# Performance work log

Hardware: AMD Instinct MI355X
Metric: run time of the kernel (lower is better)

The kernel has to match this reference:

```python
import jax, jax.numpy as jnp
import numpy as np

B, S, D, H, T, R = 2, 2048, 768, 12, 64, 50
DH = D // H
EPS = 1e-12


def setup_inputs() -> dict:
    key = jax.random.key(0)
    ks = jax.random.split(key, 12)
    w = lambda k, shape: jax.random.normal(k, shape, jnp.float32) * 0.02
    inp = {
        "hidden_states": jax.random.normal(ks[0], (B, S, D), jnp.float32),
        "tag_emb": w(ks[1], (T, D)),
        "sa_wq": w(ks[2], (D, D)), "sa_bq": jnp.zeros((D,), jnp.float32),
        "sa_wk": w(ks[3], (D, D)), "sa_bk": jnp.zeros((D,), jnp.float32),
        "sa_wv": w(ks[4], (D, D)), "sa_bv": jnp.zeros((D,), jnp.float32),
        "sa_wo": w(ks[5], (D, D)), "sa_bo": jnp.zeros((D,), jnp.float32),
        "sa_ln_g": jnp.ones((D,), jnp.float32), "sa_ln_b": jnp.zeros((D,), jnp.float32),
        "ca_wq": w(ks[6], (D, D)), "ca_bq": jnp.zeros((D,), jnp.float32),
        "ca_wk": w(ks[7], (D, D)), "ca_bk": jnp.zeros((D,), jnp.float32),
        "ca_wv": w(ks[8], (D, D)), "ca_bv": jnp.zeros((D,), jnp.float32),
        "ca_wo": w(ks[9], (D, D)), "ca_bo": jnp.zeros((D,), jnp.float32),
        "ca_ln_g": jnp.ones((D,), jnp.float32), "ca_ln_b": jnp.zeros((D,), jnp.float32),
        "ff_w1": w(ks[10], (D, 3072)), "ff_b1": jnp.zeros((3072,), jnp.float32),
        "ff_w2": w(ks[11], (3072, D)), "ff_b2": jnp.zeros((D,), jnp.float32),
        "ff_ln_g": jnp.ones((D,), jnp.float32), "ff_ln_b": jnp.zeros((D,), jnp.float32),
    }
    return inp


def _layernorm(x, g, b):
    m = jnp.mean(x, axis=-1, keepdims=True)
    v = jnp.mean(jnp.square(x - m), axis=-1, keepdims=True)
    return (x - m) * jax.lax.rsqrt(v + EPS) * g + b


def _bert_attention(x, kv, mask, wq, bq, wk, bk, wv, bv, wo, bo, ln_g, ln_b):
    # BertSelfAttention: multi-head attn; mask (if any) is ADDED to scores (HF semantics).
    Bq, Sq = x.shape[0], x.shape[1]
    Sk = kv.shape[1]
    q = (x @ wq + bq).reshape(Bq, Sq, H, DH)
    k = (kv @ wk + bk).reshape(Bq, Sk, H, DH)
    v = (kv @ wv + bv).reshape(Bq, Sk, H, DH)
    scores = jnp.einsum("bqhd,bkhd->bhqk", q, k) / jnp.sqrt(jnp.float32(DH))
    if mask is not None:
        scores = scores + mask  # additive 0/1 band mask, as in the source
    probs = jax.nn.softmax(scores, axis=-1)
    ctx = jnp.einsum("bhqk,bkhd->bqhd", probs, v).reshape(Bq, Sq, D)
    # BertSelfOutput: dense + residual + LayerNorm
    return _layernorm(ctx @ wo + bo + x, ln_g, ln_b)


def reference(hidden_states, tag_emb,
              sa_wq, sa_bq, sa_wk, sa_bk, sa_wv, sa_bv, sa_wo, sa_bo, sa_ln_g, sa_ln_b,
              ca_wq, ca_bq, ca_wk, ca_bk, ca_wv, ca_bv, ca_wo, ca_bo, ca_ln_g, ca_ln_b,
              ff_w1, ff_b1, ff_w2, ff_b2, ff_ln_g, ff_ln_b):
    Sd = hidden_states.shape[1]
    # banded mask: tril(+R) * triu(-R) -> 1 inside window, 0 outside (added to scores)
    i = jnp.arange(Sd)
    band = (jnp.abs(i[:, None] - i[None, :]) <= R).astype(hidden_states.dtype)  # [S,S]
    attn_out = _bert_attention(hidden_states, hidden_states, band,
                               sa_wq, sa_bq, sa_wk, sa_bk, sa_wv, sa_bv,
                               sa_wo, sa_bo, sa_ln_g, sa_ln_b)
    tags = jnp.broadcast_to(tag_emb[None], (hidden_states.shape[0], T, D))
    attn_out = _bert_attention(attn_out, tags, None,
                               ca_wq, ca_bq, ca_wk, ca_bk, ca_wv, ca_bv,
                               ca_wo, ca_bo, ca_ln_g, ca_ln_b)
    # BertIntermediate + BertOutput (exact erf gelu as in HF)
    inter = jax.nn.gelu(attn_out @ ff_w1 + ff_b1, approximate=False)
    return _layernorm(inter @ ff_w2 + ff_b2 + attn_out, ff_ln_g, ff_ln_b)
```

## Files before the change

kernel.cpp:

```cpp
#include <hip/hip_runtime.h>
#include <cstdint>
#include <cstddef>


typedef __bf16 bf16;
typedef __bf16 bf16x8 __attribute__((ext_vector_type(8)));
typedef __bf16 bf16x4 __attribute__((ext_vector_type(4)));
typedef __bf16 bf16x2 __attribute__((ext_vector_type(2)));
typedef float  floatx4 __attribute__((ext_vector_type(4)));

__device__ __forceinline__ void glds16(const bf16* g, bf16* l) {
  __builtin_amdgcn_global_load_lds((const __attribute__((address_space(1))) void*)g,
                                   (__attribute__((address_space(3))) void*)l, 16, 0, 0);
}

__device__ __forceinline__ float fexp2(float x) {
  float r;
  asm("v_exp_f32 %0, %1" : "=v"(r) : "v"(x));
  return r;
}

__global__ __launch_bounds__(256) void k_prep_all(const float* __restrict__ sa_bq,
                                                  const float* __restrict__ sa_bk,
                                                  const float* __restrict__ sa_bv,
                                                  const float* __restrict__ ca_bk,
                                                  const float* __restrict__ ca_bv,
                                                  const float* __restrict__ tag,
                                                  const float* __restrict__ X,
                                                  float* __restrict__ bQKV,
                                                  float* __restrict__ bKV2,
                                                  bf16* __restrict__ tagp,
                                                  bf16* __restrict__ Xb) {
  int b = blockIdx.x, t = threadIdx.x;
  if (b < 9) {
    int i = b * 256 + t;
    int s = i / 768, j = i - s * 768;
    const float* p = s == 0 ? sa_bq : (s == 1 ? sa_bk : sa_bv);
    bQKV[i] = p[j];
  } else if (b < 15) {
    int i = (b - 9) * 256 + t;
    int s = i / 768, j = i - s * 768;
    bKV2[i] = s == 0 ? ca_bk[j] : ca_bv[j];
  } else if (b < 399) {
    int i = (b - 15) * 256 + t;
    if (i < 64 * 768) tagp[i] = (bf16)tag[i];
    else tagp[i] = (bf16)0.f;
  } else {
    int i = ((b - 399) * 256 + t) * 8;
    float4 a = *(const float4*)(X + i);
    float4 b4 = *(const float4*)(X + i + 4);
    bf16x8 o;
    o[0] = (bf16)a.x; o[1] = (bf16)a.y; o[2] = (bf16)a.z; o[3] = (bf16)a.w;
    o[4] = (bf16)b4.x; o[5] = (bf16)b4.y; o[6] = (bf16)b4.z; o[7] = (bf16)b4.w;
    *(bf16x8*)(Xb + i) = o;
  }
}

__device__ __forceinline__ void transpose_body(const float* __restrict__ W,
                                               bf16* __restrict__ Wt,
                                               int K, int N, int n0, int k0,
                                               bf16 (*tile)[72]) {
  int t = threadIdx.x;
  int r = t >> 2, cg = (t & 3) * 16;
  const float* src = W + (size_t)(k0 + r) * N + n0 + cg;
  float tmp[16];
  *(float4*)&tmp[0]  = *(const float4*)(src);
  *(float4*)&tmp[4]  = *(const float4*)(src + 4);
  *(float4*)&tmp[8]  = *(const float4*)(src + 8);
  *(float4*)&tmp[12] = *(const float4*)(src + 12);
#pragma unroll
  for (int i = 0; i < 16; ++i) tile[r][cg + i] = (bf16)tmp[i];
  __syncthreads();
  bf16* dst = Wt + (size_t)(n0 + r) * K + k0 + cg;
#pragma unroll
  for (int g = 0; g < 2; ++g) {
    bf16x8 pack;
#pragma unroll
    for (int i = 0; i < 8; ++i) pack[i] = tile[cg + g * 8 + i][r];
    *(bf16x8*)(dst + g * 8) = pack;
  }
}

__global__ __launch_bounds__(256) void k_transpose4(const float* __restrict__ W0,
                                                    const float* __restrict__ W1,
                                                    const float* __restrict__ W2w,
                                                    const float* __restrict__ W3,
                                                    bf16* __restrict__ Wt) {
  __shared__ bf16 tile[64][72];
  int z = blockIdx.z;
  const float* W = z == 0 ? W0 : (z == 1 ? W1 : (z == 2 ? W2w : W3));
  transpose_body(W, Wt + (size_t)z * 768 * 768, 768, 768,
                 blockIdx.x * 64, blockIdx.y * 64, tile);
}

__global__ __launch_bounds__(256) void k_transpose_ff(const float* __restrict__ ff_w1,
                                                      const float* __restrict__ ff_w2,
                                                      bf16* __restrict__ Wall,
                                                      bf16* __restrict__ W2) {
  __shared__ bf16 tile[64][72];
  if (blockIdx.z == 0)
    transpose_body(ff_w1, Wall, 768, 3072, blockIdx.x * 64, blockIdx.y * 64, tile);
  else
    transpose_body(ff_w2, W2, 3072, 768, blockIdx.y * 64, blockIdx.x * 64, tile);
}

template <int BM, int BN, int KS, bool CF32>
__device__ __forceinline__ void gemm_body(const bf16* __restrict__ Ab,
                                          const bf16* __restrict__ Bt,
                                          const float* __restrict__ bias,
                                          void* __restrict__ Co,
                                          int N, int K, int ld, int act,
                                          int m0, int n0,
                                          bf16* __restrict__ As,
                                          bf16* __restrict__ Bs) {
  constexpr int MT = BM / 32;
  constexpr int NT = BN / 32;
  int tid = threadIdx.x;
  int lane = tid & 63, wave = tid >> 6;
  int l16 = lane & 15, quad = lane >> 4;
  int wm = wave & 1, wn = wave >> 1;
  int arow = tid >> 2, acol = (tid & 3) * 8;
  int ldst = arow * 32 + acol;

  const bf16* Ap = Ab + (size_t)(m0 + arow) * ld + acol;
  const bf16* Bp = Bt + (size_t)(n0 + arow) * ld + acol;

  floatx4 acc[MT][NT];
#pragma unroll
  for (int i = 0; i < MT; ++i)
#pragma unroll
    for (int j = 0; j < NT; ++j) acc[i][j] = floatx4{0.f, 0.f, 0.f, 0.f};

  for (int k = 0; k < K; k += 32 * KS) {
    __syncthreads();
#pragma unroll
    for (int ks = 0; ks < KS; ++ks) {
      glds16(Bp + k + ks * 32, Bs + ks * BN * 32 + ldst);
      if constexpr (BN == 128) glds16(Bp + (size_t)64 * ld + k + ks * 32, Bs + ks * BN * 32 + ldst + 2048);
      glds16(Ap + k + ks * 32, As + ks * BM * 32 + ldst);
      if constexpr (BM == 128) glds16(Ap + (size_t)64 * ld + k + ks * 32, As + ks * BM * 32 + ldst + 2048);
    }
    __syncthreads();
#pragma unroll
    for (int ks = 0; ks < KS; ++ks) {
      bf16x8 a_frag[MT], b_frag[NT];
#pragma unroll
      for (int mt = 0; mt < MT; ++mt)
        a_frag[mt] = *(const bf16x8*)(As + ks * BM * 32 + (wm * (BM / 2) + mt * 16 + l16) * 32 + quad * 8);
#pragma unroll
      for (int nt = 0; nt < NT; ++nt)
        b_frag[nt] = *(const bf16x8*)(Bs + ks * BN * 32 + (wn * (BN / 2) + nt * 16 + l16) * 32 + quad * 8);
#pragma unroll
      for (int mt = 0; mt < MT; ++mt)
#pragma unroll
        for (int nt = 0; nt < NT; ++nt)
          acc[mt][nt] = __builtin_amdgcn_mfma_f32_16x16x32_bf16(a_frag[mt], b_frag[nt], acc[mt][nt], 0, 0, 0);
    }
  }

#pragma unroll
  for (int nt = 0; nt < NT; ++nt) {
    int col = n0 + wn * (BN / 2) + nt * 16 + l16;
    float bv = bias ? bias[col] : 0.f;
#pragma unroll
    for (int mt = 0; mt < MT; ++mt) {
#pragma unroll
      for (int r = 0; r < 4; ++r) {
        int row = m0 + wm * (BM / 2) + mt * 16 + quad * 4 + r;
        float v = acc[mt][nt][r] + bv;
        if (act) v = 0.5f * v * (1.f + erff(v * 0.70710678118654752f));
        if constexpr (CF32) ((float*)Co)[(size_t)row * N + col] = v;
        else ((bf16*)Co)[(size_t)row * N + col] = (bf16)v;
      }
    }
  }
}

template <int BM, int BN, int KS, bool CF32>
__global__ __launch_bounds__(256) void k_gemm(const bf16* __restrict__ Ab,
                                              const bf16* __restrict__ Bt,
                                              const float* __restrict__ bias,
                                              void* __restrict__ Cv,
                                              void* __restrict__ Cv2,
                                              int N, int K, int ld, int act) {
  __shared__ bf16 As[KS * BM * 32];
  __shared__ bf16 Bs[KS * BN * 32];
  int z = blockIdx.z;
  gemm_body<BM, BN, KS, CF32>(Ab + z * K, Bt + z * K, z == 0 ? bias : nullptr,
                              z == 0 ? Cv : Cv2, N, K, ld, act,
                              blockIdx.x * BM, blockIdx.y * BN, As, Bs);
}

__global__ __launch_bounds__(256) void k_gemm_q2kv(const bf16* __restrict__ A0,
                                                   const bf16* __restrict__ B0,
                                                   const float* __restrict__ bias0,
                                                   bf16* __restrict__ C0,
                                                   const bf16* __restrict__ A1,
                                                   const bf16* __restrict__ B1,
                                                   const float* __restrict__ bias1,
                                                   bf16* __restrict__ C1) {
  __shared__ bf16 As[4 * 64 * 32];
  __shared__ bf16 Bs[4 * 64 * 32];
  if (blockIdx.z == 0) {
    gemm_body<64, 64, 4, false>(A0, B0, bias0, C0, 768, 768, 768, 0,
                                blockIdx.x * 64, blockIdx.y * 64, As, Bs);
  } else {
    if (blockIdx.y != 0 || blockIdx.x >= 48) return;
    gemm_body<64, 64, 4, false>(A1, B1, bias1, C1, 1536, 768, 768, 0,
                                (blockIdx.x & 1) * 64, (blockIdx.x >> 1) * 64, As, Bs);
  }
}

__global__ __launch_bounds__(256) void k_attn_mfma(const bf16* __restrict__ Q, int ldq,
                                                   const bf16* __restrict__ Kp,
                                                   const bf16* __restrict__ Vp, int ldkv,
                                                   bf16* __restrict__ O,
                                                   int S, int Skv,
                                                   long long kv_bstride, int bandR) {
  const int NH = 12;
  int qt = blockIdx.x, bh = blockIdx.y;
  int bb = bh / NH, h = bh % NH;
  const bf16* Qb = Q + (size_t)bb * S * ldq + h * 64;
  const bf16* Kb = Kp + (size_t)bb * kv_bstride + h * 64;
  const bf16* Vb = Vp + (size_t)bb * kv_bstride + h * 64;
  bf16* Ob = O + (size_t)bb * S * 768 + h * 64;

  __shared__ __align__(16) char smem[47104];
  float* Obuf = (float*)smem;
  float* l0_arr = (float*)(smem + 16896);

  int tid = threadIdx.x, wave = tid >> 6, lane = tid & 63;
  int quad = lane >> 4, l16 = lane & 15;
  int qh = wave & 1, kh = wave >> 1;
  bf16 (*Psw)[40] = (bf16(*)[40])(smem + 36864 + wave * 2560);

  const float C1 = 0.18033688f;
  const float C2 = 1.44269504f;

  int r = tid >> 2, cg = (tid & 3) * 16;
  int vk0 = 2 * (tid & 31);
  int vd0 = 8 * (tid >> 5);
  int vcol = (vk0 + 16 * (vd0 >> 4)) & 63;

  bf16x8 aq[2][2];
#pragma unroll
  for (int mt = 0; mt < 2; ++mt) {
    const bf16* qsrc = Qb + (size_t)(qt * 64 + qh * 32 + mt * 16 + l16) * ldq;
#pragma unroll
    for (int ks = 0; ks < 2; ++ks) {
      bf16x8 t = *(const bf16x8*)(qsrc + ks * 32 + quad * 8);
#pragma unroll
      for (int e = 0; e < 8; ++e) t[e] = (bf16)((float)t[e] * C1);
      aq[mt][ks] = t;
    }
  }

  bf16x8 kr0, kr1, vr0, vr1;
  {
    const bf16* ksrc = Kb + (size_t)r * ldkv + cg;
    kr0 = *(const bf16x8*)ksrc;
    kr1 = *(const bf16x8*)(ksrc + 8);
    const bf16* vsrc = Vb + (size_t)vk0 * ldkv + vd0;
    vr0 = *(const bf16x8*)vsrc;
    vr1 = *(const bf16x8*)(vsrc + ldkv);
  }

  float l_part[2][4];
  floatx4 acc[2][4];
#pragma unroll
  for (int mt = 0; mt < 2; ++mt)
#pragma unroll
    for (int j = 0; j < 4; ++j) {
      l_part[mt][j] = 0.f;
      acc[mt][j] = floatx4{0.f, 0.f, 0.f, 0.f};
    }

  int qi0 = qt * 64 + qh * 32 + quad * 4;

  for (int kc = 0; kc < Skv; kc += 64) {
    int cur = (kc >> 6) & 1;
    bf16 (*Ks)[72] = (bf16(*)[72])(smem + cur * 9216);
    bf16 (*Vt)[72] = (bf16(*)[72])(smem + 18432 + cur * 9216);
    *(bf16x8*)&Ks[r][cg] = kr0;
    *(bf16x8*)&Ks[r][cg + 8] = kr1;
#pragma unroll
    for (int e = 0; e < 8; ++e) {
      bf16x2 p; p[0] = vr0[e]; p[1] = vr1[e];
      *(bf16x2*)&Vt[vd0 + e][vcol] = p;
    }
    if (kc + 64 < Skv) {
      const bf16* ksrc = Kb + (size_t)(kc + 64 + r) * ldkv + cg;
      kr0 = *(const bf16x8*)ksrc;
      kr1 = *(const bf16x8*)(ksrc + 8);
      const bf16* vsrc = Vb + (size_t)(kc + 64 + vk0) * ldkv + vd0;
      vr0 = *(const bf16x8*)vsrc;
      vr1 = *(const bf16x8*)(vsrc + ldkv);
    }
    __syncthreads();

    floatx4 s[2][2];
    __builtin_amdgcn_s_setprio(1);
#pragma unroll
    for (int kt = 0; kt < 2; ++kt) {
      bf16x8 bk0 = *(const bf16x8*)&Ks[kh * 32 + kt * 16 + l16][quad * 8];
      bf16x8 bk1 = *(const bf16x8*)&Ks[kh * 32 + kt * 16 + l16][32 + quad * 8];
#pragma unroll
      for (int mt = 0; mt < 2; ++mt) {
        floatx4 c = {0.f, 0.f, 0.f, 0.f};
        c = __builtin_amdgcn_mfma_f32_16x16x32_bf16(aq[mt][0], bk0, c, 0, 0, 0);
        c = __builtin_amdgcn_mfma_f32_16x16x32_bf16(aq[mt][1], bk1, c, 0, 0, 0);
        s[mt][kt] = c;
      }
    }
    __builtin_amdgcn_s_setprio(0);

    bool masked = (bandR >= 0) && (kc <= qt * 64 + 63 + bandR) &&
                  (kc + 63 >= qt * 64 - bandR);
    if (masked) {
#pragma unroll
      for (int kt = 0; kt < 2; ++kt) {
        int kj = kc + kh * 32 + kt * 16 + l16;
        int colp = (kt * 16 + l16 + 8 * quad) & 31;
#pragma unroll
        for (int mt = 0; mt < 2; ++mt)
#pragma unroll
          for (int rr = 0; rr < 4; ++rr) {
            int d = qi0 + mt * 16 + rr - kj; if (d < 0) d = -d;
            float e = fexp2(s[mt][kt][rr] + (d <= bandR ? C2 : 0.f));
            l_part[mt][rr] += e;
            Psw[mt * 16 + quad * 4 + rr][colp] = (bf16)e;
          }
      }
    } else {
#pragma unroll
      for (int kt = 0; kt < 2; ++kt) {
        int colp = (kt * 16 + l16 + 8 * quad) & 31;
#pragma unroll
        for (int mt = 0; mt < 2; ++mt)
#pragma unroll
          for (int rr = 0; rr < 4; ++rr) {
            float e = fexp2(s[mt][kt][rr]);
            l_part[mt][rr] += e;
            Psw[mt * 16 + quad * 4 + rr][colp] = (bf16)e;
          }
      }
    }

    bf16x8 ap[2];
#pragma unroll
    for (int mt = 0; mt < 2; ++mt)
      ap[mt] = *(const bf16x8*)&Psw[mt * 16 + l16][8 * ((quad + (l16 >> 2)) & 3)];
    __builtin_amdgcn_s_setprio(1);
#pragma unroll
    for (int nt = 0; nt < 4; ++nt) {
      bf16x8 bv = *(const bf16x8*)&Vt[nt * 16 + l16][(kh * 32 + quad * 8 + 16 * nt) & 63];
#pragma unroll
      for (int mt = 0; mt < 2; ++mt)
        acc[mt][nt] = __builtin_amdgcn_mfma_f32_16x16x32_bf16(ap[mt], bv, acc[mt][nt], 0, 0, 0);
    }
    __builtin_amdgcn_s_setprio(0);
  }

  float lr[2][4];
#pragma unroll
  for (int mt = 0; mt < 2; ++mt)
#pragma unroll
    for (int rr = 0; rr < 4; ++rr) {
      float t = l_part[mt][rr];
      t += __shfl_xor(t, 1);
      t += __shfl_xor(t, 2);
      t += __shfl_xor(t, 4);
      t += __shfl_xor(t, 8);
      lr[mt][rr] = t;
    }
  __syncthreads();
  if (kh == 0) {
#pragma unroll
    for (int mt = 0; mt < 2; ++mt)
#pragma unroll
      for (int nt = 0; nt < 4; ++nt)
#pragma unroll
        for (int rr = 0; rr < 4; ++rr)
          Obuf[(qh * 32 + mt * 16 + quad * 4 + rr) * 66 + nt * 16 + l16] = acc[mt][nt][rr];
    if (l16 == 0) {
#pragma unroll
      for (int mt = 0; mt < 2; ++mt)
#pragma unroll
        for (int rr = 0; rr < 4; ++rr)
          l0_arr[qh * 32 + mt * 16 + quad * 4 + rr] = lr[mt][rr];
    }
  }
  __syncthreads();
  if (kh == 1) {
#pragma unroll
    for (int mt = 0; mt < 2; ++mt)
#pragma unroll
      for (int rr = 0; rr < 4; ++rr) {
        int ql = qh * 32 + mt * 16 + quad * 4 + rr;
        float lt = lr[mt][rr] + l0_arr[ql];
        int qrow = qt * 64 + ql;
#pragma unroll
        for (int nt = 0; nt < 4; ++nt) {
          float o = (acc[mt][nt][rr] + Obuf[ql * 66 + nt * 16 + l16]) / lt;
          Ob[(size_t)qrow * 768 + nt * 16 + l16] = (bf16)o;
        }
      }
  }
}

template <typename TY, typename TR, typename TO>
__global__ __launch_bounds__(256) void k_add_ln(const TY* __restrict__ Y,
                                                const TR* __restrict__ X,
                                                const float* __restrict__ Y2,
                                                const float* __restrict__ g,
                                                const float* __restrict__ b,
                                                TO* __restrict__ out) {
  int wave = threadIdx.x >> 6, lane = threadIdx.x & 63;
  int row = blockIdx.x * 4 + wave;
  const TY* y = Y + (size_t)row * 768;
  const TR* x = X + (size_t)row * 768;
  float v[12];
  float s = 0.f, s2 = 0.f;
#pragma unroll
  for (int c = 0; c < 3; ++c) {
    int idx = c * 256 + lane * 4;
    float yv[4], xv[4];
    if constexpr (__is_same(TY, float)) {
      float4 t = *(const float4*)(y + idx);
      yv[0] = t.x; yv[1] = t.y; yv[2] = t.z; yv[3] = t.w;
    } else {
      bf16x4 t = *(const bf16x4*)(y + idx);
#pragma unroll
      for (int i = 0; i < 4; ++i) yv[i] = (float)t[i];
    }
    if constexpr (__is_same(TR, float)) {
      float4 t = *(const float4*)(x + idx);
      xv[0] = t.x; xv[1] = t.y; xv[2] = t.z; xv[3] = t.w;
    } else {
      bf16x4 t = *(const bf16x4*)(x + idx);
#pragma unroll
      for (int i = 0; i < 4; ++i) xv[i] = (float)t[i];
    }
    if (Y2 != nullptr) {
      float4 t2 = *(const float4*)(Y2 + (size_t)row * 768 + idx);
      xv[0] += t2.x; xv[1] += t2.y; xv[2] += t2.z; xv[3] += t2.w;
    }
#pragma unroll
    for (int i = 0; i < 4; ++i) {
      float t = yv[i] + xv[i];
      v[c * 4 + i] = t; s += t; s2 += t * t;
    }
  }
#pragma unroll
  for (int off = 32; off > 0; off >>= 1) { s += __shfl_xor(s, off); s2 += __shfl_xor(s2, off); }
  float mean = s * (1.f / 768.f);
  float var = fmaxf(s2 * (1.f / 768.f) - mean * mean, 0.f);
  float inv = rsqrtf(var + 1e-12f);
  TO* o = out + (size_t)row * 768;
#pragma unroll
  for (int c = 0; c < 3; ++c) {
    int idx = c * 256 + lane * 4;
    float4 gv = *(const float4*)(g + idx);
    float4 bv = *(const float4*)(b + idx);
    float r0 = (v[c * 4 + 0] - mean) * inv * gv.x + bv.x;
    float r1 = (v[c * 4 + 1] - mean) * inv * gv.y + bv.y;
    float r2 = (v[c * 4 + 2] - mean) * inv * gv.z + bv.z;
    float r3 = (v[c * 4 + 3] - mean) * inv * gv.w + bv.w;
    if constexpr (__is_same(TO, float)) {
      float4 ov = {r0, r1, r2, r3};
      *(float4*)(o + idx) = ov;
    } else {
      bf16x4 ov;
      ov[0] = (bf16)r0; ov[1] = (bf16)r1; ov[2] = (bf16)r2; ov[3] = (bf16)r3;
      *(bf16x4*)(o + idx) = ov;
    }
  }
}

extern "C" void kernel_launch(void* const* d_in, const int* in_sizes, int n_in,
                              void* d_out, int out_size, void* d_ws, size_t ws_size,
                              hipStream_t stream) {
  (void)in_sizes; (void)n_in; (void)out_size; (void)ws_size;
  const float* X     = (const float*)d_in[0];
  const float* tag   = (const float*)d_in[1];
  const float* sa_wq = (const float*)d_in[2];
  const float* sa_bq = (const float*)d_in[3];
  const float* sa_wk = (const float*)d_in[4];
  const float* sa_bk = (const float*)d_in[5];
  const float* sa_wv = (const float*)d_in[6];
  const float* sa_bv = (const float*)d_in[7];
  const float* sa_wo = (const float*)d_in[8];
  const float* sa_bo = (const float*)d_in[9];
  const float* sa_lg = (const float*)d_in[10];
  const float* sa_lb = (const float*)d_in[11];
  const float* ca_wq = (const float*)d_in[12];
  const float* ca_bq = (const float*)d_in[13];
  const float* ca_wk = (const float*)d_in[14];
  const float* ca_bk = (const float*)d_in[15];
  const float* ca_wv = (const float*)d_in[16];
  const float* ca_bv = (const float*)d_in[17];
  const float* ca_wo = (const float*)d_in[18];
  const float* ca_bo = (const float*)d_in[19];
  const float* ca_lg = (const float*)d_in[20];
  const float* ca_lb = (const float*)d_in[21];
  const float* ff_w1 = (const float*)d_in[22];
  const float* ff_b1 = (const float*)d_in[23];
  const float* ff_w2 = (const float*)d_in[24];
  const float* ff_b2 = (const float*)d_in[25];
  const float* ff_lg = (const float*)d_in[26];
  const float* ff_lb = (const float*)d_in[27];

  float* outf = (float*)d_out;
  bf16* outb = (bf16*)d_out;
  const size_t SLOT = (size_t)4096 * 768;

  bf16* BIG   = (bf16*)d_ws;
  bf16* slotA = BIG + (size_t)4096 * 2304;
  bf16* Wall  = slotA + SLOT;
  bf16* W2    = Wall + (size_t)3072 * 768;
  bf16* tagp  = W2;
  bf16* k2v2  = W2 + (size_t)128 * 768;
  float* bQKV = (float*)(W2 + (size_t)128 * 768 + (size_t)128 * 1536);
  float* bKV2 = bQKV + 2304;
  float* P1   = (float*)(BIG + 2 * SLOT);
  bf16*  Xb   = outb + SLOT;

  dim3 blk(256);

  k_prep_all<<<dim3(1935), blk, 0, stream>>>(sa_bq, sa_bk, sa_bv, ca_bk, ca_bv, tag, X,
                                             bQKV, bKV2, tagp, Xb);

  k_transpose4<<<dim3(12, 12, 4), blk, 0, stream>>>(sa_wq, sa_wk, sa_wv, sa_wo, Wall);
  k_gemm<128, 64, 2, false><<<dim3(32, 36), blk, 0, stream>>>(Xb, Wall, bQKV, BIG, nullptr,
                                                              2304, 768, 768, 0);
  k_attn_mfma<<<dim3(32, 24), blk, 0, stream>>>(BIG, 2304, BIG + 768, BIG + 1536, 2304,
                                                outb, 2048, 2048, (long long)2048 * 2304, 50);
  k_gemm<64, 64, 4, false><<<dim3(64, 12), blk, 0, stream>>>(outb, Wall + (size_t)2304 * 768,
                                                             sa_bo, slotA, nullptr,
                                                             768, 768, 768, 0);
  k_transpose4<<<dim3(12, 12, 4), blk, 0, stream>>>(ca_wq, ca_wk, ca_wv, ca_wo, Wall);
  k_add_ln<bf16, float, bf16><<<dim3(1024), blk, 0, stream>>>(slotA, X, nullptr, sa_lg, sa_lb, slotA);

  k_gemm_q2kv<<<dim3(64, 12, 2), blk, 0, stream>>>(slotA, Wall, ca_bq, BIG,
                                                   tagp, Wall + (size_t)768 * 768, bKV2, k2v2);
  k_attn_mfma<<<dim3(32, 24), blk, 0, stream>>>(BIG, 768, k2v2, k2v2 + 768, 1536,
                                                outb, 2048, 64, 0, -1);
  k_gemm<64, 64, 4, false><<<dim3(64, 12), blk, 0, stream>>>(outb, Wall + (size_t)2304 * 768,
                                                             ca_bo, BIG + SLOT, nullptr,
                                                             768, 768, 768, 0);
  k_add_ln<bf16, bf16, bf16><<<dim3(1024), blk, 0, stream>>>(BIG + SLOT, slotA, nullptr,
                                                             ca_lg, ca_lb, slotA);

  k_transpose_ff<<<dim3(48, 12, 2), blk, 0, stream>>>(ff_w1, ff_w2, Wall, W2);
  for (int mc = 0; mc < 2; ++mc) {
    const bf16* a2 = slotA + (size_t)mc * 2048 * 768;
    float* yo = outf + (size_t)mc * 2048 * 768;
    k_gemm<128, 64, 2, false><<<dim3(16, 48), blk, 0, stream>>>(a2, Wall, ff_b1, BIG, nullptr,
                                                                3072, 768, 768, 1);
    k_gemm<64, 64, 4, true><<<dim3(32, 12, 2), blk, 0, stream>>>(BIG, W2, ff_b2, yo, P1,
                                                                 768, 1536, 3072, 0);
    k_add_ln<float, bf16, float><<<dim3(512), blk, 0, stream>>>(yo, a2, P1, ff_lg, ff_lb, yo);
  }
}
```

Before: 387.4 us.

## Double-buffer GEMM shared-memory tiles to overlap global loads with MFMA

Restructures the GEMM main loop into a ping-pong scheme: the next K-slab is issued via global_load_lds into the alternate LDS buffer while MFMAs run on the current one, so only one barrier is needed per iteration. To keep LDS usage the same, the 64x64 GEMMs drop from KS=4 to KS=2 per stage. The aim is to hide global-load latency behind compute, at the cost of more iterations per tile and reliance on the barrier correctly ordering the async LDS writes against reads.

```diff
diff --git a/kernel.cpp b/kernel.cpp
--- a/kernel.cpp
+++ b/kernel.cpp
@@ -115,6 +115,7 @@
                                           bf16* __restrict__ Bs) {
   constexpr int MT = BM / 32;
   constexpr int NT = BN / 32;
+  constexpr int KSTEP = 32 * KS;
   int tid = threadIdx.x;
   int lane = tid & 63, wave = tid >> 6;
   int l16 = lane & 15, quad = lane >> 4;
@@ -125,37 +126,49 @@
   const bf16* Ap = Ab + (size_t)(m0 + arow) * ld + acol;
   const bf16* Bp = Bt + (size_t)(n0 + arow) * ld + acol;
 
+  auto stage = [&](int k, int buf) {
+    bf16* Asb = As + buf * (KS * BM * 32);
+    bf16* Bsb = Bs + buf * (KS * BN * 32);
+#pragma unroll
+    for (int ks = 0; ks < KS; ++ks) {
+      glds16(Bp + k + ks * 32, Bsb + ks * BN * 32 + ldst);
+      if constexpr (BN == 128) glds16(Bp + (size_t)64 * ld + k + ks * 32, Bsb + ks * BN * 32 + ldst + 2048);
+      glds16(Ap + k + ks * 32, Asb + ks * BM * 32 + ldst);
+      if constexpr (BM == 128) glds16(Ap + (size_t)64 * ld + k + ks * 32, Asb + ks * BM * 32 + ldst + 2048);
+    }
+  };
+
   floatx4 acc[MT][NT];
 #pragma unroll
   for (int i = 0; i < MT; ++i)
 #pragma unroll
     for (int j = 0; j < NT; ++j) acc[i][j] = floatx4{0.f, 0.f, 0.f, 0.f};
 
-  for (int k = 0; k < K; k += 32 * KS) {
-    __syncthreads();
-#pragma unroll
-    for (int ks = 0; ks < KS; ++ks) {
-      glds16(Bp + k + ks * 32, Bs + ks * BN * 32 + ldst);
-      if constexpr (BN == 128) glds16(Bp + (size_t)64 * ld + k + ks * 32, Bs + ks * BN * 32 + ldst + 2048);
-      glds16(Ap + k + ks * 32, As + ks * BM * 32 + ldst);
-      if constexpr (BM == 128) glds16(Ap + (size_t)64 * ld + k + ks * 32, As + ks * BM * 32 + ldst + 2048);
-    }
-    __syncthreads();
+  stage(0, 0);
+  __syncthreads();
+
+  int cur = 0;
+  for (int k = 0; k < K; k += KSTEP) {
+    if (k + KSTEP < K) stage(k + KSTEP, cur ^ 1);
+    bf16* Asb = As + cur * (KS * BM * 32);
+    bf16* Bsb = Bs + cur * (KS * BN * 32);
 #pragma unroll
     for (int ks = 0; ks < KS; ++ks) {
       bf16x8 a_frag[MT], b_frag[NT];
 #pragma unroll
       for (int mt = 0; mt < MT; ++mt)
-        a_frag[mt] = *(const bf16x8*)(As + ks * BM * 32 + (wm * (BM / 2) + mt * 16 + l16) * 32 + quad * 8);
+        a_frag[mt] = *(const bf16x8*)(Asb + ks * BM * 32 + (wm * (BM / 2) + mt * 16 + l16) * 32 + quad * 8);
 #pragma unroll
       for (int nt = 0; nt < NT; ++nt)
-        b_frag[nt] = *(const bf16x8*)(Bs + ks * BN * 32 + (wn * (BN / 2) + nt * 16 + l16) * 32 + quad * 8);
+        b_frag[nt] = *(const bf16x8*)(Bsb + ks * BN * 32 + (wn * (BN / 2) + nt * 16 + l16) * 32 + quad * 8);
 #pragma unroll
       for (int mt = 0; mt < MT; ++mt)
 #pragma unroll
         for (int nt = 0; nt < NT; ++nt)
           acc[mt][nt] = __builtin_amdgcn_mfma_f32_16x16x32_bf16(a_frag[mt], b_frag[nt], acc[mt][nt], 0, 0, 0);
     }
+    __syncthreads();
+    cur ^= 1;
   }
 
 #pragma unroll
@@ -183,8 +196,8 @@
                                               void* __restrict__ Cv,
                                               void* __restrict__ Cv2,
                                               int N, int K, int ld, int act) {
-  __shared__ bf16 As[KS * BM * 32];
-  __shared__ bf16 Bs[KS * BN * 32];
+  __shared__ bf16 As[2 * KS * BM * 32];
+  __shared__ bf16 Bs[2 * KS * BN * 32];
   int z = blockIdx.z;
   gemm_body<BM, BN, KS, CF32>(Ab + z * K, Bt + z * K, z == 0 ? bias : nullptr,
                               z == 0 ? Cv : Cv2, N, K, ld, act,
@@ -199,14 +212,14 @@
                                                    const bf16* __restrict__ B1,
                                                    const float* __restrict__ bias1,
                                                    bf16* __restrict__ C1) {
-  __shared__ bf16 As[4 * 64 * 32];
-  __shared__ bf16 Bs[4 * 64 * 32];
+  __shared__ bf16 As[2 * 2 * 64 * 32];
+  __shared__ bf16 Bs[2 * 2 * 64 * 32];
   if (blockIdx.z == 0) {
-    gemm_body<64, 64, 4, false>(A0, B0, bias0, C0, 768, 768, 768, 0,
+    gemm_body<64, 64, 2, false>(A0, B0, bias0, C0, 768, 768, 768, 0,
                                 blockIdx.x * 64, blockIdx.y * 64, As, Bs);
   } else {
     if (blockIdx.y != 0 || blockIdx.x >= 48) return;
-    gemm_body<64, 64, 4, false>(A1, B1, bias1, C1, 1536, 768, 768, 0,
+    gemm_body<64, 64, 2, false>(A1, B1, bias1, C1, 1536, 768, 768, 0,
                                 (blockIdx.x & 1) * 64, (blockIdx.x >> 1) * 64, As, Bs);
   }
 }
@@ -535,7 +548,7 @@
                                                               2304, 768, 768, 0);
   k_attn_mfma<<<dim3(32, 24), blk, 0, stream>>>(BIG, 2304, BIG + 768, BIG + 1536, 2304,
                                                 outb, 2048, 2048, (long long)2048 * 2304, 50);
-  k_gemm<64, 64, 4, false><<<dim3(64, 12), blk, 0, stream>>>(outb, Wall + (size_t)2304 * 768,
+  k_gemm<64, 64, 2, false><<<dim3(64, 12), blk, 0, stream>>>(outb, Wall + (size_t)2304 * 768,
                                                              sa_bo, slotA, nullptr,
                                                              768, 768, 768, 0);
   k_transpose4<<<dim3(12, 12, 4), blk, 0, stream>>>(ca_wq, ca_wk, ca_wv, ca_wo, Wall);
@@ -545,7 +558,7 @@
                                                    tagp, Wall + (size_t)768 * 768, bKV2, k2v2);
   k_attn_mfma<<<dim3(32, 24), blk, 0, stream>>>(BIG, 768, k2v2, k2v2 + 768, 1536,
                                                 outb, 2048, 64, 0, -1);
-  k_gemm<64, 64, 4, false><<<dim3(64, 12), blk, 0, stream>>>(outb, Wall + (size_t)2304 * 768,
+  k_gemm<64, 64, 2, false><<<dim3(64, 12), blk, 0, stream>>>(outb, Wall + (size_t)2304 * 768,
                                                              ca_bo, BIG + SLOT, nullptr,
                                                              768, 768, 768, 0);
   k_add_ln<bf16, bf16, bf16><<<dim3(1024), blk, 0, stream>>>(BIG + SLOT, slotA, nullptr,
@@ -557,7 +570,7 @@
     float* yo = outf + (size_t)mc * 2048 * 768;
     k_gemm<128, 64, 2, false><<<dim3(16, 48), blk, 0, stream>>>(a2, Wall, ff_b1, BIG, nullptr,
                                                                 3072, 768, 768, 1);
-    k_gemm<64, 64, 4, true><<<dim3(32, 12, 2), blk, 0, stream>>>(BIG, W2, ff_b2, yo, P1,
+    k_gemm<64, 64, 2, true><<<dim3(32, 12, 2), blk, 0, stream>>>(BIG, W2, ff_b2, yo, P1,
                                                                  768, 1536, 3072, 0);
     k_add_ln<float, bf16, float><<<dim3(512), blk, 0, stream>>>(yo, a2, P1, ff_lg, ff_lb, yo);
   }
```

New measurement: 386.0 us. No clear change (-0.4%).
